# Kernel optimization log

Measured on AMD Instinct MI355X. Metric: run time of the kernel, lower is better.

Reference implementation:

```python
import jax, jax.numpy as jnp
import numpy as np

D, N, K = 6, 32768, 16          # depths, nodes per depth, max children
V, DIN, DOUT = 100000, 64, 64   # vocab, embed dim, hidden dim


def setup_inputs() -> dict:
    key = jax.random.key(0)
    ks = jax.random.split(key, 6)
    labels = jax.random.randint(ks[0], (D, N), 0, V, dtype=jnp.int32)
    # child index 0 == no child (masked); 1..N index previous depth's nodes
    child_idx = jax.random.randint(ks[1], (D, N, K), 0, N + 1, dtype=jnp.int32)
    E = jax.random.uniform(ks[2], (V, DIN), jnp.float32, -0.05, 0.05)
    s_in = 1.0 / np.sqrt(DIN)
    W_w = jax.random.uniform(ks[3], (DIN, 4 * DOUT), jnp.float32, -s_in, s_in)
    W_b = jnp.zeros((4 * DOUT,), jnp.float32)
    s_out = 1.0 / np.sqrt(DOUT)
    U_f = jax.random.uniform(ks[4], (DOUT, DOUT), jnp.float32, -s_out, s_out)
    U_iuo = jax.random.uniform(ks[5], (DOUT, 3 * DOUT), jnp.float32, -s_out, s_out)
    return {"labels": labels, "child_idx": child_idx, "E": E,
            "W_w": W_w, "W_b": W_b, "U_f": U_f, "U_iuo": U_iuo}


def _tree_lstm(labels, child_idx, E, W_w, W_b, U_f, U_iuo):
    d = U_f.shape[0]
    n = labels.shape[1]
    zero_row = jnp.zeros((1, d), jnp.float32)

    def step(carry, inp):
        h_prev, c_prev = carry            # [N+1, d], row 0 = zero init state
        lab, idx = inp                    # [N], [N, K]
        x = E[lab]                        # [N, din] embedding lookup
        mask = (idx != 0).astype(jnp.float32)   # [N, K]
        h = h_prev[idx]                   # [N, K, d] gather children hidden
        c = c_prev[idx]                   # [N, K, d] gather children cell
        h_sum = jnp.einsum('nkd,nk->nd', h, mask)  # masked child-sum
        Wx = x @ W_w + W_b                # [N, 4d]
        W_f_x, W_i_x, W_u_x, W_o_x = jnp.split(Wx, 4, axis=-1)
        # per-child forget gate
        f_k = jax.nn.sigmoid(W_f_x[:, None, :] + jnp.einsum('nkd,de->nke', h, U_f))
        branch_f = jnp.einsum('nkd,nkd,nk->nd', f_k, c, mask)
        iuo = h_sum @ U_iuo               # [N, 3d]
        i_g = jax.nn.sigmoid(iuo[:, :d] + W_i_x)
        u_g = jnp.tanh(iuo[:, d:2 * d] + W_u_x)
        o_g = jax.nn.sigmoid(iuo[:, 2 * d:] + W_o_x)
        new_c = i_g * u_g + branch_f
        new_h = o_g * jnp.tanh(new_c)
        h_next = jnp.concatenate([zero_row, new_h], 0)
        c_next = jnp.concatenate([zero_row, new_c], 0)
        return (h_next, c_next), None

    init = (jnp.zeros((n + 1, d), jnp.float32), jnp.zeros((n + 1, d), jnp.float32))
    (h_fin, _c_fin), _ = jax.lax.scan(step, init, (labels, child_idx))
    return h_fin[1:]                      # final-depth (roots) hidden [N, d]


def reference(labels, child_idx, E, W_w, W_b, U_f, U_iuo):
    return _tree_lstm(labels, child_idx, E, W_w, W_b, U_f, U_iuo)
```

## Files before the change

kernel.cpp:

```cpp
#include <hip/hip_runtime.h>

#define NN 32768
#define KK 16
#define DD 6

typedef short short8 __attribute__((ext_vector_type(8)));
typedef float floatx4 __attribute__((ext_vector_type(4)));
typedef _Float16 half4v __attribute__((ext_vector_type(4)));

__device__ __forceinline__ float sigm(float x) { return 1.0f / (1.0f + __expf(-x)); }
__device__ __forceinline__ float ftanh(float x) {
    float e = __expf(2.0f * x);
    return 1.0f - 2.0f / (e + 1.0f);
}
__device__ __forceinline__ unsigned short f2bf(float x) {
    union { float f; unsigned u; } v; v.f = x;
    unsigned r = v.u + 0x7FFF + ((v.u >> 16) & 1);
    return (unsigned short)(r >> 16);
}
__device__ __forceinline__ float bf2f(unsigned short h) {
    union { unsigned u; float f; } v; v.u = ((unsigned)h) << 16; return v.f;
}

__global__ __launch_bounds__(256) void k0_all(
    const int* __restrict__ labels, const float* __restrict__ E,
    const float* __restrict__ W_w, const float* __restrict__ W_b,
    _Float16* __restrict__ WxF)
{
    __shared__ int labs[64];
    __shared__ __align__(16) unsigned short Ax[64][74];
    __shared__ __align__(16) unsigned short Bw[256][74];
    const int tid = threadIdx.x;
    const int blk = blockIdx.x & 511;
    const int dep = blockIdx.x >> 9;
    const int n0 = blk * 64;
    if (tid < 64) labs[tid] = labels[(size_t)dep * NN + n0 + tid];
    __syncthreads();
    {
        const int m = tid >> 2, q = tid & 3;
        const float4* e4 = (const float4*)(E + (size_t)labs[m] * 64 + q * 16);
#pragma unroll
        for (int i = 0; i < 4; ++i) {
            float4 v = e4[i];
            Ax[m][q * 16 + i * 4 + 0] = f2bf(v.x);
            Ax[m][q * 16 + i * 4 + 1] = f2bf(v.y);
            Ax[m][q * 16 + i * 4 + 2] = f2bf(v.z);
            Ax[m][q * 16 + i * 4 + 3] = f2bf(v.w);
        }
    }
    {
        const int c = tid;
#pragma unroll 4
        for (int k = 0; k < 64; ++k) Bw[c][k] = f2bf(W_w[k * 256 + c]);
    }
    __syncthreads();
    const int ln = tid & 63, wv = tid >> 6;
    const int lr = ln & 15, qd = ln >> 4;
    short8 af[2];
#pragma unroll
    for (int ks = 0; ks < 2; ++ks)
        af[ks] = *(const short8*)&Ax[wv * 16 + lr][ks * 32 + qd * 8];
    floatx4 acc[16];
#pragma unroll
    for (int nt = 0; nt < 16; ++nt) acc[nt] = (floatx4){0.f, 0.f, 0.f, 0.f};
#pragma unroll
    for (int nt = 0; nt < 16; ++nt) {
#pragma unroll
        for (int ks = 0; ks < 2; ++ks) {
            short8 bw = *(const short8*)&Bw[nt * 16 + lr][ks * 32 + qd * 8];
            acc[nt] = __builtin_amdgcn_mfma_f32_16x16x32_bf16(af[ks], bw, acc[nt], 0, 0, 0);
        }
    }
    _Float16* __restrict__ base =
        WxF + ((size_t)(dep * 512 + blk) * 4 + wv) * 16 * 256 + (size_t)ln * 4;
#pragma unroll
    for (int nt = 0; nt < 16; ++nt) {
        const float bb = W_b[nt * 16 + lr];
        half4v hv;
#pragma unroll
        for (int r = 0; r < 4; ++r) hv[r] = (_Float16)(acc[nt][r] + bb);
        *(half4v*)&base[nt * 256] = hv;
    }
}

__global__ __launch_bounds__(256) void kd_fused(
    const int* __restrict__ cidx, const unsigned* __restrict__ sprev,
    const _Float16* __restrict__ Wx, const float* __restrict__ U_iuo,
    const float* __restrict__ U_f, unsigned* __restrict__ snext,
    float* __restrict__ out, int first, int last)
{
    __shared__ __align__(16) unsigned short Bi[192][68];
    __shared__ __align__(16) unsigned short Bf[64][68];
    __shared__ __align__(16) unsigned short Ah[64][68];
    __shared__ __align__(16) unsigned short AlHs[64][68];
    const int tid = threadIdx.x;
    const int n0 = blockIdx.x * 64;
    if (tid < 192) {
        const int c = tid;
#pragma unroll 4
        for (int k = 0; k < 64; ++k) Bi[c][k] = f2bf(U_iuo[k * 192 + c]);
    } else {
        const int c = tid - 192;
#pragma unroll 4
        for (int k = 0; k < 64; ++k) Bf[c][k] = f2bf(U_f[k * 64 + c]);
    }
    const int ln = tid & 63, wv = tid >> 6;
    const int lr = ln & 15, qd = ln >> 4;
    const _Float16* __restrict__ wbase =
        Wx + ((size_t)blockIdx.x * 4 + wv) * 16 * 256 + (size_t)ln * 4;

    float hs[4][4] = {{0.f}}, bfv[4][4] = {{0.f}};
    if (!first) {
        float wfx[4][4];
#pragma unroll
        for (int nt = 0; nt < 4; ++nt) {
            const half4v fv = *(const half4v*)&wbase[nt * 256];
#pragma unroll
            for (int r = 0; r < 4; ++r) wfx[r][nt] = (float)fv[r];
        }
        const _Float16* __restrict__ ch = (const _Float16*)sprev;
        const size_t cb = (size_t)(n0 + wv * 16 + qd * 4) * KK;
        int id[4];
#pragma unroll
        for (int r = 0; r < 4; ++r) id[r] = cidx[cb + r * KK];
#pragma unroll 1
        for (int k = 0; k < KK; ++k) {
            unsigned hg[4][4];
            _Float16 cv[4][4];
#pragma unroll
            for (int r = 0; r < 4; ++r)
#pragma unroll
                for (int nt = 0; nt < 4; ++nt)
                    hg[r][nt] = sprev[(size_t)id[r] * 96 + nt * 16 + lr];
#pragma unroll
            for (int r = 0; r < 4; ++r)
#pragma unroll
                for (int nt = 0; nt < 4; ++nt)
                    cv[r][nt] = ch[(size_t)id[r] * 192 + 128 + nt * 16 + lr];
            int idn[4];
            if (k + 1 < KK) {
#pragma unroll
                for (int r = 0; r < 4; ++r) idn[r] = cidx[cb + r * KK + k + 1];
            }
#pragma unroll
            for (int r = 0; r < 4; ++r)
#pragma unroll
                for (int nt = 0; nt < 4; ++nt) {
                    const float h = (float)(short)(hg[r][nt] & 0xFFFFu) * (1.f / 32767.f);
                    const float g = (float)((int)hg[r][nt] >> 16) * (1.f / 2048.f);
                    hs[r][nt] += h;
                    bfv[r][nt] = fmaf(sigm(wfx[r][nt] + g), (float)cv[r][nt], bfv[r][nt]);
                }
            if (k + 1 < KK) {
#pragma unroll
                for (int r = 0; r < 4; ++r) id[r] = idn[r];
            }
        }
    }
#pragma unroll
    for (int r = 0; r < 4; ++r)
#pragma unroll
        for (int nt = 0; nt < 4; ++nt) {
            const int m = wv * 16 + qd * 4 + r, col = nt * 16 + lr;
            const unsigned short hi = f2bf(hs[r][nt]);
            Ah[m][col] = hi;
            AlHs[m][col] = f2bf(hs[r][nt] - bf2f(hi));
        }
    __syncthreads();
    short8 ah[2], al[2];
#pragma unroll
    for (int ks = 0; ks < 2; ++ks) {
        ah[ks] = *(const short8*)&Ah[wv * 16 + lr][ks * 32 + qd * 8];
        al[ks] = *(const short8*)&AlHs[wv * 16 + lr][ks * 32 + qd * 8];
    }
    floatx4 acc[12];
#pragma unroll
    for (int nt = 0; nt < 12; ++nt) {
        floatx4 a = (floatx4){0.f, 0.f, 0.f, 0.f};
#pragma unroll
        for (int ks = 0; ks < 2; ++ks) {
            const short8 bu = *(const short8*)&Bi[nt * 16 + lr][ks * 32 + qd * 8];
            a = __builtin_amdgcn_mfma_f32_16x16x32_bf16(al[ks], bu, a, 0, 0, 0);
            a = __builtin_amdgcn_mfma_f32_16x16x32_bf16(ah[ks], bu, a, 0, 0, 0);
        }
        acc[nt] = a;
    }
    float nhv[4][4], ncv[4][4];
#pragma unroll
    for (int nt = 0; nt < 4; ++nt) {
        const int col = nt * 16 + lr;
        const half4v iv = *(const half4v*)&wbase[(4 + nt) * 256];
        const half4v uv = *(const half4v*)&wbase[(8 + nt) * 256];
        const half4v ov = *(const half4v*)&wbase[(12 + nt) * 256];
#pragma unroll
        for (int r = 0; r < 4; ++r) {
            const int node = n0 + wv * 16 + qd * 4 + r;
            const float ig = sigm(acc[nt][r] + (float)iv[r]);
            const float ug = ftanh(acc[4 + nt][r] + (float)uv[r]);
            const float og = sigm(acc[8 + nt][r] + (float)ov[r]);
            const float nc = fmaf(ig, ug, bfv[r][nt]);
            const float nh = og * ftanh(nc);
            nhv[nt][r] = nh;
            ncv[nt][r] = nc;
            if (last) {
                out[(size_t)node * 64 + col] = nh;
            } else {
                AlHs[wv * 16 + qd * 4 + r][col] = f2bf(nh);
            }
        }
    }
    if (!last) {
        short8 ag[2];
#pragma unroll
        for (int ks = 0; ks < 2; ++ks)
            ag[ks] = *(const short8*)&AlHs[wv * 16 + lr][ks * 32 + qd * 8];
        floatx4 g[4];
#pragma unroll
        for (int nt = 0; nt < 4; ++nt) {
            g[nt] = (floatx4){0.f, 0.f, 0.f, 0.f};
#pragma unroll
            for (int ks = 0; ks < 2; ++ks) {
                const short8 bfr = *(const short8*)&Bf[nt * 16 + lr][ks * 32 + qd * 8];
                g[nt] = __builtin_amdgcn_mfma_f32_16x16x32_bf16(ag[ks], bfr, g[nt], 0, 0, 0);
            }
        }
        _Float16* __restrict__ dh = (_Float16*)snext;
#pragma unroll
        for (int nt = 0; nt < 4; ++nt) {
#pragma unroll
            for (int r = 0; r < 4; ++r) {
                const int node = n0 + wv * 16 + qd * 4 + r;
                const int hq = (int)rintf(nhv[nt][r] * 32767.f);
                const int gq = (int)rintf(g[nt][r] * 2048.f);
                snext[(size_t)(node + 1) * 96 + nt * 16 + lr] =
                    ((unsigned)hq & 0xFFFFu) | ((unsigned)gq << 16);
                dh[(size_t)(node + 1) * 192 + 128 + nt * 16 + lr] =
                    (_Float16)ncv[nt][r];
            }
        }
        if (blockIdx.x == 0 && tid < 96)
            snext[tid] = 0u;
    }
}

extern "C" void kernel_launch(void* const* d_in, const int* in_sizes, int n_in,
                              void* d_out, int out_size, void* d_ws, size_t ws_size,
                              hipStream_t stream)
{
    const int*   labels = (const int*)d_in[0];
    const int*   child  = (const int*)d_in[1];
    const float* E      = (const float*)d_in[2];
    const float* W_w    = (const float*)d_in[3];
    const float* W_b    = (const float*)d_in[4];
    const float* U_f    = (const float*)d_in[5];
    const float* U_iuo  = (const float*)d_in[6];
    float* out = (float*)d_out;

    unsigned* s0 = (unsigned*)d_ws;
    unsigned* s1 = s0 + (size_t)(NN + 1) * 96;
    _Float16* WxF = (_Float16*)(s1 + (size_t)(NN + 1) * 96);

    k0_all<<<6 * (NN / 64), 256, 0, stream>>>(labels, E, W_w, W_b, WxF);

    unsigned* sp = s0;
    unsigned* sn = s1;
    for (int d = 0; d < DD; ++d) {
        const int last = (d == DD - 1);
        kd_fused<<<NN / 64, 256, 0, stream>>>(
            child + (size_t)d * NN * KK, sp,
            WxF + (size_t)d * NN * 256,
            U_iuo, U_f, sn, out, d == 0, last);
        unsigned* ts = sp; sp = sn; sn = ts;
    }
}
```

Measured before the change: 327.8 us.

## Compute per-child forget gate via MFMA on gathered fp16 h; prepack weights once

The new code stops precomputing U_f·h per node in the producer and storing it quantized next to h. Instead each consumer gathers child h rows as fp16 vectors (one node row per lane) and recomputes the forget-gate matmul with f16 MFMA against a shared-memory copy of U_f. Weights are converted and swizzled once into MFMA fragment order by a new prep kernel, so the per-block transpose/convert loops and most LDS staging go away. The state becomes a plain fp16 h/c layout of 128 halves per node. The trade is extra MFMA work per child, a doubled h gather (per row and per lane groups), and a higher occupancy hint.

```diff
diff --git a/kernel.cpp b/kernel.cpp
--- a/kernel.cpp
+++ b/kernel.cpp
@@ -7,6 +7,7 @@
 typedef short short8 __attribute__((ext_vector_type(8)));
 typedef float floatx4 __attribute__((ext_vector_type(4)));
 typedef _Float16 half4v __attribute__((ext_vector_type(4)));
+typedef _Float16 half8 __attribute__((ext_vector_type(8)));
 
 __device__ __forceinline__ float sigm(float x) { return 1.0f / (1.0f + __expf(-x)); }
 __device__ __forceinline__ float ftanh(float x) {
@@ -22,94 +23,101 @@
     union { unsigned u; float f; } v; v.u = ((unsigned)h) << 16; return v.f;
 }
 
+__global__ __launch_bounds__(256) void k_prep(
+    const float* __restrict__ W_w, const float* __restrict__ U_iuo,
+    const float* __restrict__ U_f,
+    unsigned short* __restrict__ WwF, unsigned short* __restrict__ BiF,
+    _Float16* __restrict__ BfF)
+{
+    const int t = blockIdx.x * 256 + threadIdx.x;
+    if (t < 16384) {
+        const int u = t, j = u & 7, ln = (u >> 3) & 63, ks = (u >> 9) & 1, nt = u >> 10;
+        const int col = nt * 16 + (ln & 15), k = ks * 32 + (ln >> 4) * 8 + j;
+        WwF[u] = f2bf(W_w[k * 256 + col]);
+    } else if (t < 28672) {
+        const int u = t - 16384, j = u & 7, ln = (u >> 3) & 63, ks = (u >> 9) & 1, nt = u >> 10;
+        const int col = nt * 16 + (ln & 15), k = ks * 32 + (ln >> 4) * 8 + j;
+        BiF[u] = f2bf(U_iuo[k * 192 + col]);
+    } else {
+        const int u = t - 28672, j = u & 7, ln = (u >> 3) & 63, ks = (u >> 9) & 1, nt = u >> 10;
+        const int col = nt * 16 + (ln & 15), k = ks * 32 + (ln >> 4) * 8 + j;
+        BfF[u] = (_Float16)U_f[k * 64 + col];
+    }
+}
+
 __global__ __launch_bounds__(256) void k0_all(
     const int* __restrict__ labels, const float* __restrict__ E,
-    const float* __restrict__ W_w, const float* __restrict__ W_b,
+    const unsigned short* __restrict__ WwF, const float* __restrict__ W_b,
     _Float16* __restrict__ WxF)
 {
-    __shared__ int labs[64];
-    __shared__ __align__(16) unsigned short Ax[64][74];
-    __shared__ __align__(16) unsigned short Bw[256][74];
     const int tid = threadIdx.x;
     const int blk = blockIdx.x & 511;
     const int dep = blockIdx.x >> 9;
     const int n0 = blk * 64;
-    if (tid < 64) labs[tid] = labels[(size_t)dep * NN + n0 + tid];
-    __syncthreads();
-    {
-        const int m = tid >> 2, q = tid & 3;
-        const float4* e4 = (const float4*)(E + (size_t)labs[m] * 64 + q * 16);
-#pragma unroll
-        for (int i = 0; i < 4; ++i) {
-            float4 v = e4[i];
-            Ax[m][q * 16 + i * 4 + 0] = f2bf(v.x);
-            Ax[m][q * 16 + i * 4 + 1] = f2bf(v.y);
-            Ax[m][q * 16 + i * 4 + 2] = f2bf(v.z);
-            Ax[m][q * 16 + i * 4 + 3] = f2bf(v.w);
-        }
-    }
-    {
-        const int c = tid;
-#pragma unroll 4
-        for (int k = 0; k < 64; ++k) Bw[c][k] = f2bf(W_w[k * 256 + c]);
-    }
-    __syncthreads();
     const int ln = tid & 63, wv = tid >> 6;
     const int lr = ln & 15, qd = ln >> 4;
+    const int lab = labels[(size_t)dep * NN + n0 + wv * 16 + lr];
+    const float4* __restrict__ e4 = (const float4*)(E + (size_t)lab * 64);
     short8 af[2];
 #pragma unroll
-    for (int ks = 0; ks < 2; ++ks)
-        af[ks] = *(const short8*)&Ax[wv * 16 + lr][ks * 32 + qd * 8];
-    floatx4 acc[16];
-#pragma unroll
-    for (int nt = 0; nt < 16; ++nt) acc[nt] = (floatx4){0.f, 0.f, 0.f, 0.f};
-#pragma unroll
-    for (int nt = 0; nt < 16; ++nt) {
-#pragma unroll
-        for (int ks = 0; ks < 2; ++ks) {
-            short8 bw = *(const short8*)&Bw[nt * 16 + lr][ks * 32 + qd * 8];
-            acc[nt] = __builtin_amdgcn_mfma_f32_16x16x32_bf16(af[ks], bw, acc[nt], 0, 0, 0);
-        }
-    }
+    for (int ks = 0; ks < 2; ++ks) {
+        const float4 v0 = e4[ks * 8 + qd * 2 + 0];
+        const float4 v1 = e4[ks * 8 + qd * 2 + 1];
+        short8 a;
+        a[0] = (short)f2bf(v0.x); a[1] = (short)f2bf(v0.y);
+        a[2] = (short)f2bf(v0.z); a[3] = (short)f2bf(v0.w);
+        a[4] = (short)f2bf(v1.x); a[5] = (short)f2bf(v1.y);
+        a[6] = (short)f2bf(v1.z); a[7] = (short)f2bf(v1.w);
+        af[ks] = a;
+    }
+    const short8* __restrict__ bw = (const short8*)WwF;
     _Float16* __restrict__ base =
         WxF + ((size_t)(dep * 512 + blk) * 4 + wv) * 16 * 256 + (size_t)ln * 4;
 #pragma unroll
     for (int nt = 0; nt < 16; ++nt) {
+        floatx4 a = (floatx4){0.f, 0.f, 0.f, 0.f};
+        a = __builtin_amdgcn_mfma_f32_16x16x32_bf16(af[0], bw[(nt * 2 + 0) * 64 + ln], a, 0, 0, 0);
+        a = __builtin_amdgcn_mfma_f32_16x16x32_bf16(af[1], bw[(nt * 2 + 1) * 64 + ln], a, 0, 0, 0);
         const float bb = W_b[nt * 16 + lr];
         half4v hv;
 #pragma unroll
-        for (int r = 0; r < 4; ++r) hv[r] = (_Float16)(acc[nt][r] + bb);
+        for (int r = 0; r < 4; ++r) hv[r] = (_Float16)(a[r] + bb);
         *(half4v*)&base[nt * 256] = hv;
     }
 }
 
-__global__ __launch_bounds__(256) void kd_fused(
-    const int* __restrict__ cidx, const unsigned* __restrict__ sprev,
-    const _Float16* __restrict__ Wx, const float* __restrict__ U_iuo,
-    const float* __restrict__ U_f, unsigned* __restrict__ snext,
+__global__ __launch_bounds__(256, 4) void kd_fused(
+    const int* __restrict__ cidx, const _Float16* __restrict__ sprev,
+    const _Float16* __restrict__ Wx, const unsigned short* __restrict__ BiF,
+    const _Float16* __restrict__ BfF, _Float16* __restrict__ snext,
     float* __restrict__ out, int first, int last)
 {
-    __shared__ __align__(16) unsigned short Bi[192][68];
-    __shared__ __align__(16) unsigned short Bf[64][68];
-    __shared__ __align__(16) unsigned short Ah[64][68];
-    __shared__ __align__(16) unsigned short AlHs[64][68];
+    __shared__ __align__(16) _Float16 BfL[4096];
     const int tid = threadIdx.x;
     const int n0 = blockIdx.x * 64;
-    if (tid < 192) {
-        const int c = tid;
-#pragma unroll 4
-        for (int k = 0; k < 64; ++k) Bi[c][k] = f2bf(U_iuo[k * 192 + c]);
-    } else {
-        const int c = tid - 192;
-#pragma unroll 4
-        for (int k = 0; k < 64; ++k) Bf[c][k] = f2bf(U_f[k * 64 + c]);
+    {
+        const half8* __restrict__ src = (const half8*)BfF;
+        half8* dst = (half8*)BfL;
+        dst[tid] = src[tid];
+        dst[tid + 256] = src[tid + 256];
     }
     const int ln = tid & 63, wv = tid >> 6;
     const int lr = ln & 15, qd = ln >> 4;
     const _Float16* __restrict__ wbase =
         Wx + ((size_t)blockIdx.x * 4 + wv) * 16 * 256 + (size_t)ln * 4;
-
-    float hs[4][4] = {{0.f}}, bfv[4][4] = {{0.f}};
+    __syncthreads();
+
+    float hsA[2][8];
+    float bfv[4][4];
+#pragma unroll
+    for (int ks = 0; ks < 2; ++ks)
+#pragma unroll
+        for (int j = 0; j < 8; ++j) hsA[ks][j] = 0.f;
+#pragma unroll
+    for (int r = 0; r < 4; ++r)
+#pragma unroll
+        for (int nt = 0; nt < 4; ++nt) bfv[r][nt] = 0.f;
+
     if (!first) {
         float wfx[4][4];
 #pragma unroll
@@ -118,74 +126,77 @@
 #pragma unroll
             for (int r = 0; r < 4; ++r) wfx[r][nt] = (float)fv[r];
         }
-        const _Float16* __restrict__ ch = (const _Float16*)sprev;
+        const size_t hb = (size_t)(n0 + wv * 16 + lr) * KK;
         const size_t cb = (size_t)(n0 + wv * 16 + qd * 4) * KK;
-        int id[4];
-#pragma unroll
-        for (int r = 0; r < 4; ++r) id[r] = cidx[cb + r * KK];
+        const half8* __restrict__ bl = (const half8*)BfL;
+        int idh = cidx[hb];
+        int idc[4];
+#pragma unroll
+        for (int r = 0; r < 4; ++r) idc[r] = cidx[cb + r * KK];
 #pragma unroll 1
         for (int k = 0; k < KK; ++k) {
-            unsigned hg[4][4];
+            const half8 hf0 = *(const half8*)&sprev[(size_t)idh * 128 + qd * 8];
+            const half8 hf1 = *(const half8*)&sprev[(size_t)idh * 128 + 32 + qd * 8];
             _Float16 cv[4][4];
 #pragma unroll
             for (int r = 0; r < 4; ++r)
 #pragma unroll
                 for (int nt = 0; nt < 4; ++nt)
-                    hg[r][nt] = sprev[(size_t)id[r] * 96 + nt * 16 + lr];
-#pragma unroll
-            for (int r = 0; r < 4; ++r)
-#pragma unroll
-                for (int nt = 0; nt < 4; ++nt)
-                    cv[r][nt] = ch[(size_t)id[r] * 192 + 128 + nt * 16 + lr];
-            int idn[4];
+                    cv[r][nt] = sprev[(size_t)idc[r] * 128 + 64 + nt * 16 + lr];
+            int idhn = 0, idcn[4];
             if (k + 1 < KK) {
-#pragma unroll
-                for (int r = 0; r < 4; ++r) idn[r] = cidx[cb + r * KK + k + 1];
-            }
-#pragma unroll
-            for (int r = 0; r < 4; ++r)
-#pragma unroll
-                for (int nt = 0; nt < 4; ++nt) {
-                    const float h = (float)(short)(hg[r][nt] & 0xFFFFu) * (1.f / 32767.f);
-                    const float g = (float)((int)hg[r][nt] >> 16) * (1.f / 2048.f);
-                    hs[r][nt] += h;
-                    bfv[r][nt] = fmaf(sigm(wfx[r][nt] + g), (float)cv[r][nt], bfv[r][nt]);
-                }
+                idhn = cidx[hb + k + 1];
+#pragma unroll
+                for (int r = 0; r < 4; ++r) idcn[r] = cidx[cb + r * KK + k + 1];
+            }
+#pragma unroll
+            for (int nt = 0; nt < 4; ++nt) {
+                floatx4 g = (floatx4){0.f, 0.f, 0.f, 0.f};
+                g = __builtin_amdgcn_mfma_f32_16x16x32_f16(hf0, bl[(nt * 2 + 0) * 64 + ln], g, 0, 0, 0);
+                g = __builtin_amdgcn_mfma_f32_16x16x32_f16(hf1, bl[(nt * 2 + 1) * 64 + ln], g, 0, 0, 0);
+#pragma unroll
+                for (int r = 0; r < 4; ++r)
+                    bfv[r][nt] = fmaf(sigm(wfx[r][nt] + g[r]), (float)cv[r][nt], bfv[r][nt]);
+            }
+#pragma unroll
+            for (int j = 0; j < 8; ++j) {
+                hsA[0][j] += (float)hf0[j];
+                hsA[1][j] += (float)hf1[j];
+            }
             if (k + 1 < KK) {
-#pragma unroll
-                for (int r = 0; r < 4; ++r) id[r] = idn[r];
-            }
-        }
-    }
-#pragma unroll
-    for (int r = 0; r < 4; ++r)
-#pragma unroll
-        for (int nt = 0; nt < 4; ++nt) {
-            const int m = wv * 16 + qd * 4 + r, col = nt * 16 + lr;
-            const unsigned short hi = f2bf(hs[r][nt]);
-            Ah[m][col] = hi;
-            AlHs[m][col] = f2bf(hs[r][nt] - bf2f(hi));
-        }
-    __syncthreads();
-    short8 ah[2], al[2];
-#pragma unroll
-    for (int ks = 0; ks < 2; ++ks) {
-        ah[ks] = *(const short8*)&Ah[wv * 16 + lr][ks * 32 + qd * 8];
-        al[ks] = *(const short8*)&AlHs[wv * 16 + lr][ks * 32 + qd * 8];
+                idh = idhn;
+#pragma unroll
+                for (int r = 0; r < 4; ++r) idc[r] = idcn[r];
+            }
+        }
     }
     floatx4 acc[12];
 #pragma unroll
-    for (int nt = 0; nt < 12; ++nt) {
-        floatx4 a = (floatx4){0.f, 0.f, 0.f, 0.f};
-#pragma unroll
-        for (int ks = 0; ks < 2; ++ks) {
-            const short8 bu = *(const short8*)&Bi[nt * 16 + lr][ks * 32 + qd * 8];
-            a = __builtin_amdgcn_mfma_f32_16x16x32_bf16(al[ks], bu, a, 0, 0, 0);
-            a = __builtin_amdgcn_mfma_f32_16x16x32_bf16(ah[ks], bu, a, 0, 0, 0);
-        }
-        acc[nt] = a;
-    }
-    float nhv[4][4], ncv[4][4];
+    for (int nt = 0; nt < 12; ++nt) acc[nt] = (floatx4){0.f, 0.f, 0.f, 0.f};
+    if (!first) {
+        short8 ahi[2], alo[2];
+#pragma unroll
+        for (int ks = 0; ks < 2; ++ks)
+#pragma unroll
+            for (int j = 0; j < 8; ++j) {
+                const float v = hsA[ks][j];
+                const unsigned short hi = f2bf(v);
+                ahi[ks][j] = (short)hi;
+                alo[ks][j] = (short)f2bf(v - bf2f(hi));
+            }
+        const short8* __restrict__ bi = (const short8*)BiF;
+#pragma unroll
+        for (int nt = 0; nt < 12; ++nt) {
+            floatx4 a = (floatx4){0.f, 0.f, 0.f, 0.f};
+#pragma unroll
+            for (int ks = 0; ks < 2; ++ks) {
+                const short8 bu = bi[(nt * 2 + ks) * 64 + ln];
+                a = __builtin_amdgcn_mfma_f32_16x16x32_bf16(alo[ks], bu, a, 0, 0, 0);
+                a = __builtin_amdgcn_mfma_f32_16x16x32_bf16(ahi[ks], bu, a, 0, 0, 0);
+            }
+            acc[nt] = a;
+        }
+    }
 #pragma unroll
     for (int nt = 0; nt < 4; ++nt) {
         const int col = nt * 16 + lr;
@@ -200,47 +211,16 @@
             const float og = sigm(acc[8 + nt][r] + (float)ov[r]);
             const float nc = fmaf(ig, ug, bfv[r][nt]);
             const float nh = og * ftanh(nc);
-            nhv[nt][r] = nh;
-            ncv[nt][r] = nc;
             if (last) {
                 out[(size_t)node * 64 + col] = nh;
             } else {
-                AlHs[wv * 16 + qd * 4 + r][col] = f2bf(nh);
-            }
-        }
-    }
-    if (!last) {
-        short8 ag[2];
-#pragma unroll
-        for (int ks = 0; ks < 2; ++ks)
-            ag[ks] = *(const short8*)&AlHs[wv * 16 + lr][ks * 32 + qd * 8];
-        floatx4 g[4];
-#pragma unroll
-        for (int nt = 0; nt < 4; ++nt) {
-            g[nt] = (floatx4){0.f, 0.f, 0.f, 0.f};
-#pragma unroll
-            for (int ks = 0; ks < 2; ++ks) {
-                const short8 bfr = *(const short8*)&Bf[nt * 16 + lr][ks * 32 + qd * 8];
-                g[nt] = __builtin_amdgcn_mfma_f32_16x16x32_bf16(ag[ks], bfr, g[nt], 0, 0, 0);
-            }
-        }
-        _Float16* __restrict__ dh = (_Float16*)snext;
-#pragma unroll
-        for (int nt = 0; nt < 4; ++nt) {
-#pragma unroll
-            for (int r = 0; r < 4; ++r) {
-                const int node = n0 + wv * 16 + qd * 4 + r;
-                const int hq = (int)rintf(nhv[nt][r] * 32767.f);
-                const int gq = (int)rintf(g[nt][r] * 2048.f);
-                snext[(size_t)(node + 1) * 96 + nt * 16 + lr] =
-                    ((unsigned)hq & 0xFFFFu) | ((unsigned)gq << 16);
-                dh[(size_t)(node + 1) * 192 + 128 + nt * 16 + lr] =
-                    (_Float16)ncv[nt][r];
-            }
-        }
-        if (blockIdx.x == 0 && tid < 96)
-            snext[tid] = 0u;
-    }
+                snext[(size_t)(node + 1) * 128 + col] = (_Float16)nh;
+                snext[(size_t)(node + 1) * 128 + 64 + col] = (_Float16)nc;
+            }
+        }
+    }
+    if (!last && blockIdx.x == 0 && tid < 64)
+        ((unsigned*)snext)[tid] = 0u;
 }
 
 extern "C" void kernel_launch(void* const* d_in, const int* in_sizes, int n_in,
@@ -256,20 +236,24 @@
     const float* U_iuo  = (const float*)d_in[6];
     float* out = (float*)d_out;
 
-    unsigned* s0 = (unsigned*)d_ws;
-    unsigned* s1 = s0 + (size_t)(NN + 1) * 96;
-    _Float16* WxF = (_Float16*)(s1 + (size_t)(NN + 1) * 96);
-
-    k0_all<<<6 * (NN / 64), 256, 0, stream>>>(labels, E, W_w, W_b, WxF);
-
-    unsigned* sp = s0;
-    unsigned* sn = s1;
+    _Float16* s0 = (_Float16*)d_ws;
+    _Float16* s1 = s0 + (size_t)(NN + 1) * 128;
+    _Float16* WxF = s1 + (size_t)(NN + 1) * 128;
+    unsigned short* WwF = (unsigned short*)(WxF + (size_t)6 * NN * 256);
+    unsigned short* BiF = WwF + 16384;
+    _Float16* BfF = (_Float16*)(BiF + 12288);
+
+    k_prep<<<128, 256, 0, stream>>>(W_w, U_iuo, U_f, WwF, BiF, BfF);
+    k0_all<<<6 * (NN / 64), 256, 0, stream>>>(labels, E, WwF, W_b, WxF);
+
+    _Float16* sp = s0;
+    _Float16* sn = s1;
     for (int d = 0; d < DD; ++d) {
         const int last = (d == DD - 1);
         kd_fused<<<NN / 64, 256, 0, stream>>>(
             child + (size_t)d * NN * KK, sp,
             WxF + (size_t)d * NN * 256,
-            U_iuo, U_f, sn, out, d == 0, last);
-        unsigned* ts = sp; sp = sn; sn = ts;
-    }
-}
+            BiF, BfF, sn, out, d == 0, last);
+        _Float16* ts = sp; sp = sn; sn = ts;
+    }
+}
```

New measurement: 427.3 us. 1.3x slower.

## Pre-swizzle bf16 weights once and split child loop across waves

Applied to the files above, without the earlier changes.

Adds a prep kernel that converts W_w, U_iuo and U_f to bf16 once, stored in MFMA fragment order. This removes the per-block transpose and convert into shared memory in both the embedding projection and the per-depth kernels, which now read B fragments straight from global memory. The per-depth kernel now gives each block 32 nodes, with two wave pairs each covering half of the 16 children; partial sums are combined through shared memory, and the second half-waves exit early. This doubles the block count to expose more parallelism in the latency-bound gather, at the cost of an extra LDS reduction, idle waves during the GEMM phase and repeated global weight reads.

```diff
diff --git a/kernel.cpp b/kernel.cpp
--- a/kernel.cpp
+++ b/kernel.cpp
@@ -22,109 +22,101 @@
     union { unsigned u; float f; } v; v.u = ((unsigned)h) << 16; return v.f;
 }
 
+__global__ __launch_bounds__(256) void k_prep(
+    const float* __restrict__ W_w, const float* __restrict__ U_iuo,
+    const float* __restrict__ U_f,
+    unsigned short* __restrict__ WwF, unsigned short* __restrict__ BiF,
+    unsigned short* __restrict__ UfF)
+{
+    const int t = blockIdx.x * 256 + threadIdx.x;
+    if (t < 16384) {
+        const int u = t, j = u & 7, ln = (u >> 3) & 63, ks = (u >> 9) & 1, nt = u >> 10;
+        const int col = nt * 16 + (ln & 15), k = ks * 32 + (ln >> 4) * 8 + j;
+        WwF[u] = f2bf(W_w[k * 256 + col]);
+    } else if (t < 28672) {
+        const int u = t - 16384, j = u & 7, ln = (u >> 3) & 63, ks = (u >> 9) & 1, nt = u >> 10;
+        const int col = nt * 16 + (ln & 15), k = ks * 32 + (ln >> 4) * 8 + j;
+        BiF[u] = f2bf(U_iuo[k * 192 + col]);
+    } else {
+        const int u = t - 28672, j = u & 7, ln = (u >> 3) & 63, ks = (u >> 9) & 1, nt = u >> 10;
+        const int col = nt * 16 + (ln & 15), k = ks * 32 + (ln >> 4) * 8 + j;
+        UfF[u] = f2bf(U_f[k * 64 + col]);
+    }
+}
+
 __global__ __launch_bounds__(256) void k0_all(
     const int* __restrict__ labels, const float* __restrict__ E,
-    const float* __restrict__ W_w, const float* __restrict__ W_b,
+    const unsigned short* __restrict__ WwF, const float* __restrict__ W_b,
     _Float16* __restrict__ WxF)
 {
-    __shared__ int labs[64];
-    __shared__ __align__(16) unsigned short Ax[64][74];
-    __shared__ __align__(16) unsigned short Bw[256][74];
     const int tid = threadIdx.x;
     const int blk = blockIdx.x & 511;
     const int dep = blockIdx.x >> 9;
     const int n0 = blk * 64;
-    if (tid < 64) labs[tid] = labels[(size_t)dep * NN + n0 + tid];
-    __syncthreads();
-    {
-        const int m = tid >> 2, q = tid & 3;
-        const float4* e4 = (const float4*)(E + (size_t)labs[m] * 64 + q * 16);
-#pragma unroll
-        for (int i = 0; i < 4; ++i) {
-            float4 v = e4[i];
-            Ax[m][q * 16 + i * 4 + 0] = f2bf(v.x);
-            Ax[m][q * 16 + i * 4 + 1] = f2bf(v.y);
-            Ax[m][q * 16 + i * 4 + 2] = f2bf(v.z);
-            Ax[m][q * 16 + i * 4 + 3] = f2bf(v.w);
-        }
-    }
-    {
-        const int c = tid;
-#pragma unroll 4
-        for (int k = 0; k < 64; ++k) Bw[c][k] = f2bf(W_w[k * 256 + c]);
-    }
-    __syncthreads();
     const int ln = tid & 63, wv = tid >> 6;
     const int lr = ln & 15, qd = ln >> 4;
+    const int lab = labels[(size_t)dep * NN + n0 + wv * 16 + lr];
+    const float4* __restrict__ e4 = (const float4*)(E + (size_t)lab * 64);
     short8 af[2];
 #pragma unroll
-    for (int ks = 0; ks < 2; ++ks)
-        af[ks] = *(const short8*)&Ax[wv * 16 + lr][ks * 32 + qd * 8];
-    floatx4 acc[16];
-#pragma unroll
-    for (int nt = 0; nt < 16; ++nt) acc[nt] = (floatx4){0.f, 0.f, 0.f, 0.f};
-#pragma unroll
-    for (int nt = 0; nt < 16; ++nt) {
-#pragma unroll
-        for (int ks = 0; ks < 2; ++ks) {
-            short8 bw = *(const short8*)&Bw[nt * 16 + lr][ks * 32 + qd * 8];
-            acc[nt] = __builtin_amdgcn_mfma_f32_16x16x32_bf16(af[ks], bw, acc[nt], 0, 0, 0);
-        }
-    }
+    for (int ks = 0; ks < 2; ++ks) {
+        const float4 v0 = e4[ks * 8 + qd * 2 + 0];
+        const float4 v1 = e4[ks * 8 + qd * 2 + 1];
+        short8 a;
+        a[0] = (short)f2bf(v0.x); a[1] = (short)f2bf(v0.y);
+        a[2] = (short)f2bf(v0.z); a[3] = (short)f2bf(v0.w);
+        a[4] = (short)f2bf(v1.x); a[5] = (short)f2bf(v1.y);
+        a[6] = (short)f2bf(v1.z); a[7] = (short)f2bf(v1.w);
+        af[ks] = a;
+    }
+    const short8* __restrict__ bw = (const short8*)WwF;
     _Float16* __restrict__ base =
         WxF + ((size_t)(dep * 512 + blk) * 4 + wv) * 16 * 256 + (size_t)ln * 4;
 #pragma unroll
     for (int nt = 0; nt < 16; ++nt) {
+        floatx4 a = (floatx4){0.f, 0.f, 0.f, 0.f};
+        a = __builtin_amdgcn_mfma_f32_16x16x32_bf16(af[0], bw[(nt * 2 + 0) * 64 + ln], a, 0, 0, 0);
+        a = __builtin_amdgcn_mfma_f32_16x16x32_bf16(af[1], bw[(nt * 2 + 1) * 64 + ln], a, 0, 0, 0);
         const float bb = W_b[nt * 16 + lr];
         half4v hv;
 #pragma unroll
-        for (int r = 0; r < 4; ++r) hv[r] = (_Float16)(acc[nt][r] + bb);
+        for (int r = 0; r < 4; ++r) hv[r] = (_Float16)(a[r] + bb);
         *(half4v*)&base[nt * 256] = hv;
     }
 }
 
-__global__ __launch_bounds__(256) void kd_fused(
+__global__ __launch_bounds__(256, 4) void kd_fused(
     const int* __restrict__ cidx, const unsigned* __restrict__ sprev,
-    const _Float16* __restrict__ Wx, const float* __restrict__ U_iuo,
-    const float* __restrict__ U_f, unsigned* __restrict__ snext,
+    const _Float16* __restrict__ Wx, const unsigned short* __restrict__ BiF,
+    const unsigned short* __restrict__ UfF, unsigned* __restrict__ snext,
     float* __restrict__ out, int first, int last)
 {
-    __shared__ __align__(16) unsigned short Bi[192][68];
-    __shared__ __align__(16) unsigned short Bf[64][68];
-    __shared__ __align__(16) unsigned short Ah[64][68];
-    __shared__ __align__(16) unsigned short AlHs[64][68];
+    __shared__ __align__(16) float comb[2][2176];
     const int tid = threadIdx.x;
-    const int n0 = blockIdx.x * 64;
-    if (tid < 192) {
-        const int c = tid;
-#pragma unroll 4
-        for (int k = 0; k < 64; ++k) Bi[c][k] = f2bf(U_iuo[k * 192 + c]);
-    } else {
-        const int c = tid - 192;
-#pragma unroll 4
-        for (int k = 0; k < 64; ++k) Bf[c][k] = f2bf(U_f[k * 64 + c]);
-    }
     const int ln = tid & 63, wv = tid >> 6;
+    const int g = wv & 1, kh = wv >> 1;
     const int lr = ln & 15, qd = ln >> 4;
+    const int n0 = blockIdx.x * 32;
     const _Float16* __restrict__ wbase =
-        Wx + ((size_t)blockIdx.x * 4 + wv) * 16 * 256 + (size_t)ln * 4;
+        Wx + ((size_t)(blockIdx.x * 2 + g)) * 4096 + (size_t)ln * 4;
 
     float hs[4][4] = {{0.f}}, bfv[4][4] = {{0.f}};
+    float wfx[4][4];
+#pragma unroll
+    for (int nt = 0; nt < 4; ++nt) {
+        const half4v fv = *(const half4v*)&wbase[nt * 256];
+#pragma unroll
+        for (int r = 0; r < 4; ++r) wfx[r][nt] = (float)fv[r];
+    }
+
     if (!first) {
-        float wfx[4][4];
-#pragma unroll
-        for (int nt = 0; nt < 4; ++nt) {
-            const half4v fv = *(const half4v*)&wbase[nt * 256];
-#pragma unroll
-            for (int r = 0; r < 4; ++r) wfx[r][nt] = (float)fv[r];
-        }
         const _Float16* __restrict__ ch = (const _Float16*)sprev;
-        const size_t cb = (size_t)(n0 + wv * 16 + qd * 4) * KK;
+        const size_t cb = (size_t)(n0 + g * 16 + qd * 4) * KK + kh * 8;
         int id[4];
 #pragma unroll
         for (int r = 0; r < 4; ++r) id[r] = cidx[cb + r * KK];
 #pragma unroll 1
-        for (int k = 0; k < KK; ++k) {
+        for (int k = 0; k < 8; ++k) {
             unsigned hg[4][4];
             _Float16 cv[4][4];
 #pragma unroll
@@ -138,7 +130,7 @@
                 for (int nt = 0; nt < 4; ++nt)
                     cv[r][nt] = ch[(size_t)id[r] * 192 + 128 + nt * 16 + lr];
             int idn[4];
-            if (k + 1 < KK) {
+            if (k + 1 < 8) {
 #pragma unroll
                 for (int r = 0; r < 4; ++r) idn[r] = cidx[cb + r * KK + k + 1];
             }
@@ -147,39 +139,65 @@
 #pragma unroll
                 for (int nt = 0; nt < 4; ++nt) {
                     const float h = (float)(short)(hg[r][nt] & 0xFFFFu) * (1.f / 32767.f);
-                    const float g = (float)((int)hg[r][nt] >> 16) * (1.f / 2048.f);
+                    const float gg = (float)((int)hg[r][nt] >> 16) * (1.f / 2048.f);
                     hs[r][nt] += h;
-                    bfv[r][nt] = fmaf(sigm(wfx[r][nt] + g), (float)cv[r][nt], bfv[r][nt]);
+                    bfv[r][nt] = fmaf(sigm(wfx[r][nt] + gg), (float)cv[r][nt], bfv[r][nt]);
                 }
-            if (k + 1 < KK) {
+            if (k + 1 < 8) {
 #pragma unroll
                 for (int r = 0; r < 4; ++r) id[r] = idn[r];
             }
         }
-    }
+        __syncthreads();
+        if (kh == 1) {
+            float* const pb = &comb[g][ln * 34];
+#pragma unroll
+            for (int r = 0; r < 4; ++r)
+#pragma unroll
+                for (int nt = 0; nt < 4; ++nt) {
+                    pb[r * 4 + nt] = hs[r][nt];
+                    pb[16 + r * 4 + nt] = bfv[r][nt];
+                }
+        }
+        __syncthreads();
+        if (kh == 0) {
+            const float* const pb = &comb[g][ln * 34];
+#pragma unroll
+            for (int r = 0; r < 4; ++r)
+#pragma unroll
+                for (int nt = 0; nt < 4; ++nt) {
+                    hs[r][nt] += pb[r * 4 + nt];
+                    bfv[r][nt] += pb[16 + r * 4 + nt];
+                }
+        }
+    }
+    if (kh != 0) return;
+
+    unsigned short* const ah_t = (unsigned short*)comb[g];
+    unsigned short* const al_t = ah_t + 16 * 68;
 #pragma unroll
     for (int r = 0; r < 4; ++r)
 #pragma unroll
         for (int nt = 0; nt < 4; ++nt) {
-            const int m = wv * 16 + qd * 4 + r, col = nt * 16 + lr;
+            const int m = qd * 4 + r, col = nt * 16 + lr;
             const unsigned short hi = f2bf(hs[r][nt]);
-            Ah[m][col] = hi;
-            AlHs[m][col] = f2bf(hs[r][nt] - bf2f(hi));
-        }
-    __syncthreads();
+            ah_t[m * 68 + col] = hi;
+            al_t[m * 68 + col] = f2bf(hs[r][nt] - bf2f(hi));
+        }
     short8 ah[2], al[2];
 #pragma unroll
     for (int ks = 0; ks < 2; ++ks) {
-        ah[ks] = *(const short8*)&Ah[wv * 16 + lr][ks * 32 + qd * 8];
-        al[ks] = *(const short8*)&AlHs[wv * 16 + lr][ks * 32 + qd * 8];
-    }
+        ah[ks] = *(const short8*)&ah_t[lr * 68 + ks * 32 + qd * 8];
+        al[ks] = *(const short8*)&al_t[lr * 68 + ks * 32 + qd * 8];
+    }
+    const short8* __restrict__ bi = (const short8*)BiF;
     floatx4 acc[12];
 #pragma unroll
     for (int nt = 0; nt < 12; ++nt) {
         floatx4 a = (floatx4){0.f, 0.f, 0.f, 0.f};
 #pragma unroll
         for (int ks = 0; ks < 2; ++ks) {
-            const short8 bu = *(const short8*)&Bi[nt * 16 + lr][ks * 32 + qd * 8];
+            const short8 bu = bi[(nt * 2 + ks) * 64 + ln];
             a = __builtin_amdgcn_mfma_f32_16x16x32_bf16(al[ks], bu, a, 0, 0, 0);
             a = __builtin_amdgcn_mfma_f32_16x16x32_bf16(ah[ks], bu, a, 0, 0, 0);
         }
@@ -194,7 +212,7 @@
         const half4v ov = *(const half4v*)&wbase[(12 + nt) * 256];
 #pragma unroll
         for (int r = 0; r < 4; ++r) {
-            const int node = n0 + wv * 16 + qd * 4 + r;
+            const int node = n0 + g * 16 + qd * 4 + r;
             const float ig = sigm(acc[nt][r] + (float)iv[r]);
             const float ug = ftanh(acc[4 + nt][r] + (float)uv[r]);
             const float og = sigm(acc[8 + nt][r] + (float)ov[r]);
@@ -205,7 +223,7 @@
             if (last) {
                 out[(size_t)node * 64 + col] = nh;
             } else {
-                AlHs[wv * 16 + qd * 4 + r][col] = f2bf(nh);
+                al_t[(qd * 4 + r) * 68 + col] = f2bf(nh);
             }
         }
     }
@@ -213,25 +231,26 @@
         short8 ag[2];
 #pragma unroll
         for (int ks = 0; ks < 2; ++ks)
-            ag[ks] = *(const short8*)&AlHs[wv * 16 + lr][ks * 32 + qd * 8];
-        floatx4 g[4];
+            ag[ks] = *(const short8*)&al_t[lr * 68 + ks * 32 + qd * 8];
+        const short8* __restrict__ bf = (const short8*)UfF;
+        floatx4 gacc[4];
 #pragma unroll
         for (int nt = 0; nt < 4; ++nt) {
-            g[nt] = (floatx4){0.f, 0.f, 0.f, 0.f};
+            gacc[nt] = (floatx4){0.f, 0.f, 0.f, 0.f};
 #pragma unroll
             for (int ks = 0; ks < 2; ++ks) {
-                const short8 bfr = *(const short8*)&Bf[nt * 16 + lr][ks * 32 + qd * 8];
-                g[nt] = __builtin_amdgcn_mfma_f32_16x16x32_bf16(ag[ks], bfr, g[nt], 0, 0, 0);
-            }
-        }
-        _Float16* __restrict__ dh = (_Float16*)snext;
+                const short8 bfr = bf[(nt * 2 + ks) * 64 + ln];
+                gacc[nt] = __builtin_amdgcn_mfma_f32_16x16x32_bf16(ag[ks], bfr, gacc[nt], 0, 0, 0);
+            }
+        }
+        _Float16* dh = (_Float16*)snext;
 #pragma unroll
         for (int nt = 0; nt < 4; ++nt) {
 #pragma unroll
             for (int r = 0; r < 4; ++r) {
-                const int node = n0 + wv * 16 + qd * 4 + r;
+                const int node = n0 + g * 16 + qd * 4 + r;
                 const int hq = (int)rintf(nhv[nt][r] * 32767.f);
-                const int gq = (int)rintf(g[nt][r] * 2048.f);
+                const int gq = (int)rintf(gacc[nt][r] * 2048.f);
                 snext[(size_t)(node + 1) * 96 + nt * 16 + lr] =
                     ((unsigned)hq & 0xFFFFu) | ((unsigned)gq << 16);
                 dh[(size_t)(node + 1) * 192 + 128 + nt * 16 + lr] =
@@ -259,17 +278,21 @@
     unsigned* s0 = (unsigned*)d_ws;
     unsigned* s1 = s0 + (size_t)(NN + 1) * 96;
     _Float16* WxF = (_Float16*)(s1 + (size_t)(NN + 1) * 96);
-
-    k0_all<<<6 * (NN / 64), 256, 0, stream>>>(labels, E, W_w, W_b, WxF);
+    unsigned short* WwF = (unsigned short*)(WxF + (size_t)6 * NN * 256);
+    unsigned short* BiF = WwF + 16384;
+    unsigned short* UfF = BiF + 12288;
+
+    k_prep<<<128, 256, 0, stream>>>(W_w, U_iuo, U_f, WwF, BiF, UfF);
+    k0_all<<<6 * (NN / 64), 256, 0, stream>>>(labels, E, WwF, W_b, WxF);
 
     unsigned* sp = s0;
     unsigned* sn = s1;
     for (int d = 0; d < DD; ++d) {
         const int last = (d == DD - 1);
-        kd_fused<<<NN / 64, 256, 0, stream>>>(
+        kd_fused<<<NN / 32, 256, 0, stream>>>(
             child + (size_t)d * NN * KK, sp,
             WxF + (size_t)d * NN * 256,
-            U_iuo, U_f, sn, out, d == 0, last);
+            BiF, UfF, sn, out, d == 0, last);
         unsigned* ts = sp; sp = sn; sn = ts;
     }
 }
```

After: 332.3 us. Within noise of the previous version (+1.4%).
